# Performance work log

Hardware: AMD Instinct MI355X
Metric: run time of the kernel (lower is better)

## Reference

```python
import math
import jax, jax.numpy as jnp
import numpy as np

N_EXPERTS = 8
N_ACTIVE = 5
N_CAMP_A = 4
TEMPERATURE = math.e


def setup_inputs() -> dict:
    key = jax.random.key(0)
    ks = jax.random.split(key, 5)
    B, T, D, I = 4, 2048, 2048, 1024
    s = 0.02
    return {
        "x": jax.random.normal(ks[0], (B, T, D), jnp.float32),
        "Wr": jax.random.normal(ks[1], (D, N_EXPERTS), jnp.float32) * s,
        "Wg": jax.random.normal(ks[2], (N_EXPERTS, D, I), jnp.float32) * s,
        "Wu": jax.random.normal(ks[3], (N_EXPERTS, D, I), jnp.float32) * s,
        "Wd": jax.random.normal(ks[4], (N_EXPERTS, I, D), jnp.float32) * s,
    }


def _router_weights(x, Wr):
    # scores: (B,T,E)
    probs = jax.nn.softmax(jnp.einsum("btd,de->bte", x, Wr) / TEMPERATURE, axis=-1)
    _, topk_idx = jax.lax.top_k(probs, N_ACTIVE)          # (B,T,k)
    mask = jax.nn.one_hot(topk_idx, N_EXPERTS, dtype=probs.dtype).sum(axis=-2)
    w = probs * mask
    return w / (w.sum(axis=-1, keepdims=True) + 1e-8)


def reference(x, Wr, Wg, Wu, Wd):
    weights = _router_weights(x, Wr)                       # (B,T,E)
    # All experts run on full dense input (faithful to source loop), batched GEMMs.
    g = jnp.einsum("btd,edi->btei", x, Wg)                 # (B,T,E,I)
    u = jnp.einsum("btd,edi->btei", x, Wu)
    h = jax.nn.silu(g) * u
    eo = jnp.einsum("btei,eid->bted", h, Wd)               # (B,T,E,D)
    sign = jnp.concatenate([jnp.ones(N_CAMP_A), -jnp.ones(N_EXPERTS - N_CAMP_A)]).astype(x.dtype)
    output = jnp.einsum("bte,bted->btd", weights * sign, eo)  # out_a - out_g
    tension_scalar = jax.lax.stop_gradient(jnp.mean(output ** 2))
    return output, tension_scalar
```

## Files before the change

### kernel.cpp

```cpp
#include <hip/hip_runtime.h>
#include <cstdint>
#include <cstddef>


typedef short bf16x8 __attribute__((ext_vector_type(8)));
typedef float f32x4 __attribute__((ext_vector_type(4)));
typedef unsigned short u16;

typedef const unsigned int __attribute__((address_space(1)))* as1_u32p;
typedef unsigned int __attribute__((address_space(3)))* as3_u32p;

#define VMCNT6 asm volatile("s_waitcnt vmcnt(6)" ::: "memory")
#define VMCNT0 asm volatile("s_waitcnt vmcnt(0)" ::: "memory")
#define LGKM0  asm volatile("s_waitcnt lgkmcnt(0)" ::: "memory")
#define SBAR   __builtin_amdgcn_s_barrier()
#define SCHED0 __builtin_amdgcn_sched_barrier(0)
#define MFMA16(af, bf, cf) __builtin_amdgcn_mfma_f32_16x16x32_bf16(af, bf, cf, 0, 0, 0)

__device__ __forceinline__ u16 f2bf(float f) {
  unsigned u = __builtin_bit_cast(unsigned, f);
  u += 0x7fffu + ((u >> 16) & 1u);
  return (u16)(u >> 16);
}

__device__ __forceinline__ void gload16(const void* g, const u16* lds) {
  as1_u32p gp = (as1_u32p)(uintptr_t)g;
  as3_u32p lp = (as3_u32p)(unsigned)(uintptr_t)lds;
  __builtin_amdgcn_global_load_lds(gp, lp, 16, 0, 0);
}

__global__ __launch_bounds__(256) void router_kernel(
    const float* __restrict__ x, const float* __restrict__ Wr,
    float* __restrict__ Cw, u16* __restrict__ Xb) {
  const int l = threadIdx.x & 63;
  const int t = blockIdx.x * 4 + (threadIdx.x >> 6);
  const float* xr = x + (size_t)t * 2048;
  u16* xbr = Xb + (size_t)t * 2048;
  float p[8] = {0.f,0.f,0.f,0.f,0.f,0.f,0.f,0.f};
#pragma unroll
  for (int it = 0; it < 8; ++it) {
    const int d0 = it * 256 + l * 4;
    const float4 xv = *(const float4*)(xr + d0);
    unsigned lo = (unsigned)f2bf(xv.x) | ((unsigned)f2bf(xv.y) << 16);
    unsigned hi = (unsigned)f2bf(xv.z) | ((unsigned)f2bf(xv.w) << 16);
    *(unsigned*)(xbr + d0) = lo;
    *(unsigned*)(xbr + d0 + 2) = hi;
    const float xs[4] = {xv.x, xv.y, xv.z, xv.w};
#pragma unroll
    for (int jj = 0; jj < 4; ++jj) {
      const float4 w0 = *(const float4*)(Wr + (size_t)(d0 + jj) * 8);
      const float4 w1 = *(const float4*)(Wr + (size_t)(d0 + jj) * 8 + 4);
      p[0] += xs[jj] * w0.x; p[1] += xs[jj] * w0.y;
      p[2] += xs[jj] * w0.z; p[3] += xs[jj] * w0.w;
      p[4] += xs[jj] * w1.x; p[5] += xs[jj] * w1.y;
      p[6] += xs[jj] * w1.z; p[7] += xs[jj] * w1.w;
    }
  }
#pragma unroll
  for (int e = 0; e < 8; ++e) {
    float v = p[e];
#pragma unroll
    for (int off = 32; off > 0; off >>= 1) v += __shfl_xor(v, off, 64);
    p[e] = v;
  }
  constexpr float INV_TEMP = 0.36787944117144233f;
  float mx = -1e30f;
#pragma unroll
  for (int e = 0; e < 8; ++e) { p[e] *= INV_TEMP; mx = fmaxf(mx, p[e]); }
  float sum = 0.f;
#pragma unroll
  for (int e = 0; e < 8; ++e) { p[e] = __expf(p[e] - mx); sum += p[e]; }
  const float inv_sum = 1.f / sum;
#pragma unroll
  for (int e = 0; e < 8; ++e) p[e] *= inv_sum;
  unsigned sel = 0xFFu;
  for (int it = 0; it < 3; ++it) {
    float mn = 1e30f; int mi = 0;
#pragma unroll
    for (int e = 0; e < 8; ++e)
      if ((sel >> e) & 1u) { if (p[e] <= mn) { mn = p[e]; mi = e; } }
    sel &= ~(1u << mi);
  }
  float wsum = 0.f;
#pragma unroll
  for (int e = 0; e < 8; ++e) if ((sel >> e) & 1u) wsum += p[e];
  const float inv_w = 1.f / (wsum + 1e-8f);
  if (l == 0) {
#pragma unroll
    for (int e = 0; e < 8; ++e) {
      float v = ((sel >> e) & 1u) ? p[e] * inv_w : 0.f;
      Cw[(size_t)t * 8 + e] = (e < 4) ? v : -v;
    }
  }
}

__global__ __launch_bounds__(256) void tcvt_kernel(
    const float* __restrict__ in, u16* __restrict__ out,
    int R, int C, long long ZO, long long CS) {
  __shared__ float tile[32][33];
  const int z = blockIdx.z;
  const float* ib = in + (size_t)z * R * C;
  const int r0 = blockIdx.y * 32, c0 = blockIdx.x * 32;
  const int tx = threadIdx.x, ty = threadIdx.y;
#pragma unroll
  for (int j = 0; j < 4; ++j)
    tile[ty + j * 8][tx] = ib[(size_t)(r0 + ty + j * 8) * C + c0 + tx];
  __syncthreads();
#pragma unroll
  for (int j = 0; j < 4; ++j)
    out[(size_t)z * ZO + (size_t)(c0 + ty + j * 8) * CS + r0 + tx] =
        f2bf(tile[tx][ty + j * 8]);
}


__global__ __launch_bounds__(512, 2) void gemm1_8p(
    const u16* __restrict__ Xb, const u16* __restrict__ Wgt,
    const u16* __restrict__ Wut, const float* __restrict__ Cw,
    u16* __restrict__ Hp, int p) {
  extern __shared__ u16 lds[];
  const int tid = threadIdx.x;
  const int l = tid & 63, w = tid >> 6;
  const int wr = w >> 2, wc = w & 3;
  const int lq = l >> 4, lr = l & 15;
  const int bid = blockIdx.x;
  const int work = (bid & 7) * 128 + (bid >> 3);
  const int mtile = work & 31;
  const int en = work >> 5;
  const int el = en >> 3, nt = en & 7;
  const int e = p * 4 + el;
  const u16* gA  = Xb + (size_t)mtile * 256 * 2048;
  const u16* s0p = Wgt + (size_t)e * 2097152 + (size_t)nt * 128 * 2048;
  const u16* s1p = Wut + (size_t)e * 2097152 + (size_t)nt * 128 * 2048;
  const u16* s2p = gA;
  const u16* s3p = gA + (size_t)128 * 2048;
  const int NT = 32;

  auto stageU = [&](int tt, const u16* srcb, int u) {
    if (tt >= NT) return;
    u16* dst = lds + (tt & 1) * 32768 + u * 8192;
    const int kt = tt * 64;
#pragma unroll
    for (int j = 0; j < 2; ++j) {
      const int g = j * 512 + tid;
      const int row = g >> 3;
      const int cg = (g & 7) ^ (row & 7);
      gload16(srcb + (size_t)row * 2048 + kt + cg * 8, dst + g * 8);
    }
  };

  const int xr = lr & 7;
  const int x0 = (lq ^ xr) * 8;
  const int x1 = ((4 + lq) ^ xr) * 8;
  const int aB = (2 + wr) * 8192 + lr * 64;
  const int gBo = (wc * 32 + lr) * 64;
  const int uBo = 8192 + (wc * 32 + lr) * 64;

  bf16x8 a[8][2], bg[2][2], bu[2][2];
  f32x4 ag[8][2], au[8][2];
#pragma unroll
  for (int mi = 0; mi < 8; ++mi)
#pragma unroll
    for (int ni = 0; ni < 2; ++ni) {
      ag[mi][ni] = (f32x4){0.f, 0.f, 0.f, 0.f};
      au[mi][ni] = (f32x4){0.f, 0.f, 0.f, 0.f};
    }

  stageU(0, s0p, 0); stageU(0, s1p, 1); stageU(0, s2p, 2); stageU(0, s3p, 3);
  stageU(1, s0p, 0); stageU(1, s1p, 1); stageU(1, s2p, 2);
  VMCNT6; SBAR;

  for (int t = 0; t < NT; ++t) {
    const u16* Lb = lds + (t & 1) * 32768;
    {
#pragma unroll
      for (int mi = 0; mi < 4; ++mi) {
        a[mi][0] = *(const bf16x8*)&Lb[aB + mi * 1024 + x0];
        a[mi][1] = *(const bf16x8*)&Lb[aB + mi * 1024 + x1];
      }
#pragma unroll
      for (int ni = 0; ni < 2; ++ni) {
        bg[ni][0] = *(const bf16x8*)&Lb[gBo + ni * 1024 + x0];
        bg[ni][1] = *(const bf16x8*)&Lb[gBo + ni * 1024 + x1];
      }
      stageU(t + 1, s3p, 3);
      SBAR; LGKM0; SCHED0;
      __builtin_amdgcn_s_setprio(1);
#pragma unroll
      for (int mi = 0; mi < 4; ++mi)
#pragma unroll
        for (int ni = 0; ni < 2; ++ni)
#pragma unroll
          for (int kk = 0; kk < 2; ++kk)
            ag[mi][ni] = MFMA16(a[mi][kk], bg[ni][kk], ag[mi][ni]);
      __builtin_amdgcn_s_setprio(0); SCHED0; SBAR;
    }
    {
#pragma unroll
      for (int ni = 0; ni < 2; ++ni) {
        bu[ni][0] = *(const bf16x8*)&Lb[uBo + ni * 1024 + x0];
        bu[ni][1] = *(const bf16x8*)&Lb[uBo + ni * 1024 + x1];
      }
      stageU(t + 2, s0p, 0);
      SBAR; LGKM0; SCHED0;
      __builtin_amdgcn_s_setprio(1);
#pragma unroll
      for (int mi = 0; mi < 4; ++mi)
#pragma unroll
        for (int ni = 0; ni < 2; ++ni)
#pragma unroll
          for (int kk = 0; kk < 2; ++kk)
            au[mi][ni] = MFMA16(a[mi][kk], bu[ni][kk], au[mi][ni]);
      __builtin_amdgcn_s_setprio(0); SCHED0; SBAR;
    }
    {
#pragma unroll
      for (int mi = 4; mi < 8; ++mi) {
        a[mi][0] = *(const bf16x8*)&Lb[aB + mi * 1024 + x0];
        a[mi][1] = *(const bf16x8*)&Lb[aB + mi * 1024 + x1];
      }
      stageU(t + 2, s1p, 1);
      SBAR; LGKM0; SCHED0;
      __builtin_amdgcn_s_setprio(1);
#pragma unroll
      for (int mi = 4; mi < 8; ++mi)
#pragma unroll
        for (int ni = 0; ni < 2; ++ni)
#pragma unroll
          for (int kk = 0; kk < 2; ++kk)
            ag[mi][ni] = MFMA16(a[mi][kk], bg[ni][kk], ag[mi][ni]);
      __builtin_amdgcn_s_setprio(0); SCHED0; SBAR;
    }
    {
      stageU(t + 2, s2p, 2);
      if (t < NT - 2) { VMCNT6; } else if (t == NT - 2) { VMCNT0; }
      SBAR; LGKM0; SCHED0;
      __builtin_amdgcn_s_setprio(1);
#pragma unroll
      for (int mi = 4; mi < 8; ++mi)
#pragma unroll
        for (int ni = 0; ni < 2; ++ni)
#pragma unroll
          for (int kk = 0; kk < 2; ++kk)
            au[mi][ni] = MFMA16(a[mi][kk], bu[ni][kk], au[mi][ni]);
      __builtin_amdgcn_s_setprio(0); SCHED0; SBAR;
    }
  }

  __syncthreads();
  float* cl = (float*)lds;
  if (tid < 256) cl[tid] = Cw[(size_t)(mtile * 256 + tid) * 8 + e];
  __syncthreads();
#pragma unroll
  for (int mi = 0; mi < 8; ++mi) {
#pragma unroll
    for (int j = 0; j < 4; ++j) {
      const int rl = wr * 128 + mi * 16 + lq * 4 + j;
      const float c = cl[rl];
      const size_t row = (size_t)mtile * 256 + rl;
#pragma unroll
      for (int ni = 0; ni < 2; ++ni) {
        const float g = ag[mi][ni][j], u = au[mi][ni][j];
        const float h = g * (1.f / (1.f + __expf(-g))) * u * c;
        Hp[row * 4096 + el * 1024 + nt * 128 + wc * 32 + ni * 16 + lr] = f2bf(h);
      }
    }
  }
}

__global__ __launch_bounds__(512, 2) void gemm2_8p(
    const u16* __restrict__ Hp, const u16* __restrict__ Wdt,
    float* __restrict__ out, int koff, int accum) {
  extern __shared__ u16 lds[];
  const int tid = threadIdx.x;
  const int l = tid & 63, w = tid >> 6;
  const int wr = w >> 2, wc = w & 3;
  const int lq = l >> 4, lr = l & 15;
  const int bid = blockIdx.x;
  const int work = (bid & 7) * 32 + (bid >> 3);
  const int mtile = work & 31, ntile = work >> 5;
  const u16* gA = Hp + (size_t)mtile * 256 * 4096;
  const u16* gB = Wdt + (size_t)ntile * 256 * 8192 + koff;
  const u16* s0p = gB;
  const u16* s1p = gB + (size_t)128 * 8192;
  const u16* s2p = gA;
  const u16* s3p = gA + (size_t)128 * 4096;
  const int NT = 64;

  auto stageU = [&](int tt, const u16* srcb, int stride, int u) {
    if (tt >= NT) return;
    u16* dst = lds + (tt & 1) * 32768 + u * 8192;
    const int kt = tt * 64;
#pragma unroll
    for (int j = 0; j < 2; ++j) {
      const int g = j * 512 + tid;
      const int row = g >> 3;
      const int cg = (g & 7) ^ (row & 7);
      gload16(srcb + (size_t)row * stride + kt + cg * 8, dst + g * 8);
    }
  };

  const int xr = lr & 7;
  const int x0 = (lq ^ xr) * 8;
  const int x1 = ((4 + lq) ^ xr) * 8;
  const int aB = (2 + wr) * 8192 + lr * 64;
  const int bB = (wc >> 1) * 8192 + ((wc & 1) * 64 + lr) * 64;

  bf16x8 a[8][2], b[4][2];
  f32x4 acc[8][4];
#pragma unroll
  for (int mi = 0; mi < 8; ++mi)
#pragma unroll
    for (int ni = 0; ni < 4; ++ni) acc[mi][ni] = (f32x4){0.f, 0.f, 0.f, 0.f};

  stageU(0, s0p, 8192, 0); stageU(0, s1p, 8192, 1);
  stageU(0, s2p, 4096, 2); stageU(0, s3p, 4096, 3);
  stageU(1, s0p, 8192, 0); stageU(1, s1p, 8192, 1); stageU(1, s2p, 4096, 2);
  VMCNT6; SBAR;

  for (int t = 0; t < NT; ++t) {
    const u16* Lb = lds + (t & 1) * 32768;
    {
#pragma unroll
      for (int mi = 0; mi < 4; ++mi) {
        a[mi][0] = *(const bf16x8*)&Lb[aB + mi * 1024 + x0];
        a[mi][1] = *(const bf16x8*)&Lb[aB + mi * 1024 + x1];
      }
#pragma unroll
      for (int ni = 0; ni < 2; ++ni) {
        b[ni][0] = *(const bf16x8*)&Lb[bB + ni * 1024 + x0];
        b[ni][1] = *(const bf16x8*)&Lb[bB + ni * 1024 + x1];
      }
      if (wc < 2) {
#pragma unroll
        for (int ni = 2; ni < 4; ++ni) {
          b[ni][0] = *(const bf16x8*)&Lb[bB + ni * 1024 + x0];
          b[ni][1] = *(const bf16x8*)&Lb[bB + ni * 1024 + x1];
        }
      }
      stageU(t + 1, s3p, 4096, 3);
      SBAR; LGKM0; SCHED0;
      __builtin_amdgcn_s_setprio(1);
#pragma unroll
      for (int mi = 0; mi < 4; ++mi)
#pragma unroll
        for (int ni = 0; ni < 2; ++ni)
#pragma unroll
          for (int kk = 0; kk < 2; ++kk)
            acc[mi][ni] = MFMA16(a[mi][kk], b[ni][kk], acc[mi][ni]);
      __builtin_amdgcn_s_setprio(0); SCHED0; SBAR;
    }
    {
      if (wc >= 2) {
#pragma unroll
        for (int ni = 2; ni < 4; ++ni) {
          b[ni][0] = *(const bf16x8*)&Lb[bB + ni * 1024 + x0];
          b[ni][1] = *(const bf16x8*)&Lb[bB + ni * 1024 + x1];
        }
      }
      stageU(t + 2, s0p, 8192, 0);
      SBAR; LGKM0; SCHED0;
      __builtin_amdgcn_s_setprio(1);
#pragma unroll
      for (int mi = 0; mi < 4; ++mi)
#pragma unroll
        for (int ni = 2; ni < 4; ++ni)
#pragma unroll
          for (int kk = 0; kk < 2; ++kk)
            acc[mi][ni] = MFMA16(a[mi][kk], b[ni][kk], acc[mi][ni]);
      __builtin_amdgcn_s_setprio(0); SCHED0; SBAR;
    }
    {
#pragma unroll
      for (int mi = 4; mi < 8; ++mi) {
        a[mi][0] = *(const bf16x8*)&Lb[aB + mi * 1024 + x0];
        a[mi][1] = *(const bf16x8*)&Lb[aB + mi * 1024 + x1];
      }
      stageU(t + 2, s1p, 8192, 1);
      SBAR; LGKM0; SCHED0;
      __builtin_amdgcn_s_setprio(1);
#pragma unroll
      for (int mi = 4; mi < 8; ++mi)
#pragma unroll
        for (int ni = 2; ni < 4; ++ni)
#pragma unroll
          for (int kk = 0; kk < 2; ++kk)
            acc[mi][ni] = MFMA16(a[mi][kk], b[ni][kk], acc[mi][ni]);
      __builtin_amdgcn_s_setprio(0); SCHED0; SBAR;
    }
    {
      stageU(t + 2, s2p, 4096, 2);
      if (t < NT - 2) { VMCNT6; } else if (t == NT - 2) { VMCNT0; }
      SBAR; LGKM0; SCHED0;
      __builtin_amdgcn_s_setprio(1);
#pragma unroll
      for (int mi = 4; mi < 8; ++mi)
#pragma unroll
        for (int ni = 0; ni < 2; ++ni)
#pragma unroll
          for (int kk = 0; kk < 2; ++kk)
            acc[mi][ni] = MFMA16(a[mi][kk], b[ni][kk], acc[mi][ni]);
      __builtin_amdgcn_s_setprio(0); SCHED0; SBAR;
    }
  }

#pragma unroll
  for (int mi = 0; mi < 8; ++mi)
#pragma unroll
    for (int ni = 0; ni < 4; ++ni)
#pragma unroll
      for (int j = 0; j < 4; ++j) {
        const int row = mtile * 256 + wr * 128 + mi * 16 + lq * 4 + j;
        const int col = ntile * 256 + wc * 64 + ni * 16 + lr;
        const size_t idx = (size_t)row * 2048 + col;
        float v = acc[mi][ni][j];
        if (accum) v += out[idx];
        out[idx] = v;
      }
}

__global__ __launch_bounds__(256) void sqsum_partial(
    const float* __restrict__ out, float* __restrict__ part, int n4) {
  float s = 0.f;
  const int idx = blockIdx.x * 256 + threadIdx.x;
  const int stride = gridDim.x * 256;
  for (int i = idx; i < n4; i += stride) {
    const float4 v = ((const float4*)out)[i];
    s += v.x * v.x + v.y * v.y + v.z * v.z + v.w * v.w;
  }
#pragma unroll
  for (int off = 32; off > 0; off >>= 1) s += __shfl_down(s, off, 64);
  __shared__ float ls[4];
  if ((threadIdx.x & 63) == 0) ls[threadIdx.x >> 6] = s;
  __syncthreads();
  if (threadIdx.x == 0) part[blockIdx.x] = ls[0] + ls[1] + ls[2] + ls[3];
}

__global__ __launch_bounds__(256) void sqsum_final(
    const float* __restrict__ part, float* __restrict__ dst, int np, float scale) {
  float s = 0.f;
  for (int i = threadIdx.x; i < np; i += 256) s += part[i];
#pragma unroll
  for (int off = 32; off > 0; off >>= 1) s += __shfl_down(s, off, 64);
  __shared__ float ls[4];
  if ((threadIdx.x & 63) == 0) ls[threadIdx.x >> 6] = s;
  __syncthreads();
  if (threadIdx.x == 0) dst[0] = (ls[0] + ls[1] + ls[2] + ls[3]) * scale;
}

extern "C" void kernel_launch(void* const* d_in, const int* in_sizes, int n_in,
                              void* d_out, int out_size, void* d_ws, size_t ws_size,
                              hipStream_t stream) {
  (void)in_sizes; (void)n_in; (void)out_size; (void)ws_size;
  const float* x  = (const float*)d_in[0];
  const float* Wr = (const float*)d_in[1];
  const float* Wg = (const float*)d_in[2];
  const float* Wu = (const float*)d_in[3];
  const float* Wd = (const float*)d_in[4];
  float* out = (float*)d_out;
  char* ws = (char*)d_ws;
  u16*   Xb   = (u16*)(ws);
  u16*   Wgt  = (u16*)(ws + 33554432);
  u16*   Wut  = (u16*)(ws + 67108864);
  u16*   Wdt  = (u16*)(ws + 100663296);
  u16*   Hp   = (u16*)(ws + 134217728);
  float* Cw   = (float*)(ws + 201326592);
  float* part = (float*)(ws + 201588736);

  (void)hipFuncSetAttribute((const void*)gemm1_8p,
                            hipFuncAttributeMaxDynamicSharedMemorySize, 131072);
  (void)hipFuncSetAttribute((const void*)gemm2_8p,
                            hipFuncAttributeMaxDynamicSharedMemorySize, 131072);

  router_kernel<<<2048, 256, 0, stream>>>(x, Wr, Cw, Xb);

  dim3 tb(32, 8);
  tcvt_kernel<<<dim3(32, 64, 8), tb, 0, stream>>>(Wg, Wgt, 2048, 1024, 2097152LL, 2048LL);
  tcvt_kernel<<<dim3(32, 64, 8), tb, 0, stream>>>(Wu, Wut, 2048, 1024, 2097152LL, 2048LL);
  tcvt_kernel<<<dim3(64, 32, 8), tb, 0, stream>>>(Wd, Wdt, 1024, 2048, 1024LL, 8192LL);

  for (int p = 0; p < 2; ++p) {
    gemm1_8p<<<1024, 512, 131072, stream>>>(Xb, Wgt, Wut, Cw, Hp, p);
    gemm2_8p<<<256, 512, 131072, stream>>>(Hp, Wdt, out, p * 4096, p);
  }

  sqsum_partial<<<1024, 256, 0, stream>>>(out, part, 16777216 / 4);
  sqsum_final<<<1, 256, 0, stream>>>(part, out + 16777216, 1024, 1.f / 16777216.f);
}
```

Before: 884.6 us.

## Gather only routed tokens per expert in gate/up GEMM

A new build_idx kernel compacts, for each expert, the list of tokens whose routing weight is nonzero. The gate/up GEMM then gathers only those token rows and exits early for tiles past the per-expert count, so the work for tokens routed elsewhere (3 of 8 experts) is skipped. To keep the dense down-projection GEMM correct, the intermediate buffer is zeroed with a memset before each phase. The staging address math is also precomputed per thread. The sparse path turns on only when the workspace is large enough, and it adds memset traffic plus gathered, less regular A-row loads.

```diff
diff --git a/kernel.cpp b/kernel.cpp
--- a/kernel.cpp
+++ b/kernel.cpp
@@ -15,6 +15,8 @@
 #define LGKM0  asm volatile("s_waitcnt lgkmcnt(0)" ::: "memory")
 #define SBAR   __builtin_amdgcn_s_barrier()
 #define SCHED0 __builtin_amdgcn_sched_barrier(0)
+#define PRIO1  __builtin_amdgcn_s_setprio(1)
+#define PRIO0  __builtin_amdgcn_s_setprio(0)
 #define MFMA16(af, bf, cf) __builtin_amdgcn_mfma_f32_16x16x32_bf16(af, bf, cf, 0, 0, 0)
 
 __device__ __forceinline__ u16 f2bf(float f) {
@@ -94,6 +96,32 @@
   }
 }
 
+__global__ __launch_bounds__(256) void build_idx(
+    const float* __restrict__ Cw, int* __restrict__ idx, int* __restrict__ cnt) {
+  const int e = blockIdx.x;
+  const int tid = threadIdx.x;
+  const int t0 = tid * 32;
+  int c = 0;
+#pragma unroll
+  for (int j = 0; j < 32; ++j)
+    if (Cw[(size_t)(t0 + j) * 8 + e] != 0.f) ++c;
+  __shared__ int s[256];
+  s[tid] = c;
+  __syncthreads();
+  for (int off = 1; off < 256; off <<= 1) {
+    int v = (tid >= off) ? s[tid - off] : 0;
+    __syncthreads();
+    s[tid] += v;
+    __syncthreads();
+  }
+  int o = e * 8192 + s[tid] - c;
+  for (int j = 0; j < 32; ++j) {
+    const int t = t0 + j;
+    if (Cw[(size_t)t * 8 + e] != 0.f) idx[o++] = t;
+  }
+  if (tid == 255) cnt[e] = s[255];
+}
+
 __global__ __launch_bounds__(256) void tcvt_kernel(
     const float* __restrict__ in, u16* __restrict__ out,
     int R, int C, long long ZO, long long CS) {
@@ -116,7 +144,8 @@
 __global__ __launch_bounds__(512, 2) void gemm1_8p(
     const u16* __restrict__ Xb, const u16* __restrict__ Wgt,
     const u16* __restrict__ Wut, const float* __restrict__ Cw,
-    u16* __restrict__ Hp, int p) {
+    u16* __restrict__ Hp, const int* __restrict__ idx,
+    const int* __restrict__ cnt, int p) {
   extern __shared__ u16 lds[];
   const int tid = threadIdx.x;
   const int l = tid & 63, w = tid >> 6;
@@ -128,24 +157,43 @@
   const int en = work >> 5;
   const int el = en >> 3, nt = en & 7;
   const int e = p * 4 + el;
-  const u16* gA  = Xb + (size_t)mtile * 256 * 2048;
+  const int cnt_e = idx ? cnt[e] : 8192;
+  const int base = mtile * 256;
+  if (base >= cnt_e) return;
+  const int* idxp = idx ? idx + (size_t)e * 8192 : nullptr;
+
   const u16* s0p = Wgt + (size_t)e * 2097152 + (size_t)nt * 128 * 2048;
   const u16* s1p = Wut + (size_t)e * 2097152 + (size_t)nt * 128 * 2048;
-  const u16* s2p = gA;
-  const u16* s3p = gA + (size_t)128 * 2048;
+
+  const int lrow = tid >> 3;
+  const int cgo = ((tid & 7) ^ (lrow & 7)) * 8;
+  const int offB0 = lrow * 2048 + cgo;
+  const int offB1 = offB0 + 64 * 2048;
+  const int d0e = tid * 8, d1e = (512 + tid) * 8;
+
+  auto gr = [&](int r) -> size_t {
+    const int rr = r < cnt_e ? r : cnt_e - 1;
+    return (size_t)(idxp ? idxp[rr] : rr) * 2048 + cgo;
+  };
+  const size_t a20 = gr(base + lrow);
+  const size_t a21 = gr(base + 64 + lrow);
+  const size_t a30 = gr(base + 128 + lrow);
+  const size_t a31 = gr(base + 192 + lrow);
+
   const int NT = 32;
-
-  auto stageU = [&](int tt, const u16* srcb, int u) {
+  auto stageB = [&](int tt, const u16* srcb, int u) {
     if (tt >= NT) return;
     u16* dst = lds + (tt & 1) * 32768 + u * 8192;
     const int kt = tt * 64;
-#pragma unroll
-    for (int j = 0; j < 2; ++j) {
-      const int g = j * 512 + tid;
-      const int row = g >> 3;
-      const int cg = (g & 7) ^ (row & 7);
-      gload16(srcb + (size_t)row * 2048 + kt + cg * 8, dst + g * 8);
-    }
+    gload16(srcb + offB0 + kt, dst + d0e);
+    gload16(srcb + offB1 + kt, dst + d1e);
+  };
+  auto stageA = [&](int tt, size_t b0, size_t b1, int u) {
+    if (tt >= NT) return;
+    u16* dst = lds + (tt & 1) * 32768 + u * 8192;
+    const int kt = tt * 64;
+    gload16(Xb + b0 + kt, dst + d0e);
+    gload16(Xb + b1 + kt, dst + d1e);
   };
 
   const int xr = lr & 7;
@@ -165,8 +213,9 @@
       au[mi][ni] = (f32x4){0.f, 0.f, 0.f, 0.f};
     }
 
-  stageU(0, s0p, 0); stageU(0, s1p, 1); stageU(0, s2p, 2); stageU(0, s3p, 3);
-  stageU(1, s0p, 0); stageU(1, s1p, 1); stageU(1, s2p, 2);
+  stageB(0, s0p, 0); stageB(0, s1p, 1);
+  stageA(0, a20, a21, 2); stageA(0, a30, a31, 3);
+  stageB(1, s0p, 0); stageB(1, s1p, 1); stageA(1, a20, a21, 2);
   VMCNT6; SBAR;
 
   for (int t = 0; t < NT; ++t) {
@@ -182,9 +231,9 @@
         bg[ni][0] = *(const bf16x8*)&Lb[gBo + ni * 1024 + x0];
         bg[ni][1] = *(const bf16x8*)&Lb[gBo + ni * 1024 + x1];
       }
-      stageU(t + 1, s3p, 3);
-      SBAR; LGKM0; SCHED0;
-      __builtin_amdgcn_s_setprio(1);
+      stageA(t + 1, a30, a31, 3);
+      SBAR; LGKM0; SCHED0;
+      PRIO1;
 #pragma unroll
       for (int mi = 0; mi < 4; ++mi)
 #pragma unroll
@@ -192,7 +241,7 @@
 #pragma unroll
           for (int kk = 0; kk < 2; ++kk)
             ag[mi][ni] = MFMA16(a[mi][kk], bg[ni][kk], ag[mi][ni]);
-      __builtin_amdgcn_s_setprio(0); SCHED0; SBAR;
+      PRIO0; SCHED0; SBAR;
     }
     {
 #pragma unroll
@@ -200,9 +249,9 @@
         bu[ni][0] = *(const bf16x8*)&Lb[uBo + ni * 1024 + x0];
         bu[ni][1] = *(const bf16x8*)&Lb[uBo + ni * 1024 + x1];
       }
-      stageU(t + 2, s0p, 0);
-      SBAR; LGKM0; SCHED0;
-      __builtin_amdgcn_s_setprio(1);
+      stageB(t + 2, s0p, 0);
+      SBAR; LGKM0; SCHED0;
+      PRIO1;
 #pragma unroll
       for (int mi = 0; mi < 4; ++mi)
 #pragma unroll
@@ -210,7 +259,7 @@
 #pragma unroll
           for (int kk = 0; kk < 2; ++kk)
             au[mi][ni] = MFMA16(a[mi][kk], bu[ni][kk], au[mi][ni]);
-      __builtin_amdgcn_s_setprio(0); SCHED0; SBAR;
+      PRIO0; SCHED0; SBAR;
     }
     {
 #pragma unroll
@@ -218,9 +267,9 @@
         a[mi][0] = *(const bf16x8*)&Lb[aB + mi * 1024 + x0];
         a[mi][1] = *(const bf16x8*)&Lb[aB + mi * 1024 + x1];
       }
-      stageU(t + 2, s1p, 1);
-      SBAR; LGKM0; SCHED0;
-      __builtin_amdgcn_s_setprio(1);
+      stageB(t + 2, s1p, 1);
+      SBAR; LGKM0; SCHED0;
+      PRIO1;
 #pragma unroll
       for (int mi = 4; mi < 8; ++mi)
 #pragma unroll
@@ -228,13 +277,13 @@
 #pragma unroll
           for (int kk = 0; kk < 2; ++kk)
             ag[mi][ni] = MFMA16(a[mi][kk], bg[ni][kk], ag[mi][ni]);
-      __builtin_amdgcn_s_setprio(0); SCHED0; SBAR;
-    }
-    {
-      stageU(t + 2, s2p, 2);
+      PRIO0; SCHED0; SBAR;
+    }
+    {
+      stageA(t + 2, a20, a21, 2);
       if (t < NT - 2) { VMCNT6; } else if (t == NT - 2) { VMCNT0; }
       SBAR; LGKM0; SCHED0;
-      __builtin_amdgcn_s_setprio(1);
+      PRIO1;
 #pragma unroll
       for (int mi = 4; mi < 8; ++mi)
 #pragma unroll
@@ -242,26 +291,26 @@
 #pragma unroll
           for (int kk = 0; kk < 2; ++kk)
             au[mi][ni] = MFMA16(a[mi][kk], bu[ni][kk], au[mi][ni]);
-      __builtin_amdgcn_s_setprio(0); SCHED0; SBAR;
-    }
-  }
-
-  __syncthreads();
-  float* cl = (float*)lds;
-  if (tid < 256) cl[tid] = Cw[(size_t)(mtile * 256 + tid) * 8 + e];
-  __syncthreads();
+      PRIO0; SCHED0; SBAR;
+    }
+  }
+
 #pragma unroll
   for (int mi = 0; mi < 8; ++mi) {
 #pragma unroll
     for (int j = 0; j < 4; ++j) {
       const int rl = wr * 128 + mi * 16 + lq * 4 + j;
-      const float c = cl[rl];
-      const size_t row = (size_t)mtile * 256 + rl;
-#pragma unroll
-      for (int ni = 0; ni < 2; ++ni) {
-        const float g = ag[mi][ni][j], u = au[mi][ni][j];
-        const float h = g * (1.f / (1.f + __expf(-g))) * u * c;
-        Hp[row * 4096 + el * 1024 + nt * 128 + wc * 32 + ni * 16 + lr] = f2bf(h);
+      const int grow = base + rl;
+      if (grow < cnt_e) {
+        const int orow = idxp ? idxp[grow] : grow;
+        const float c = Cw[(size_t)orow * 8 + e];
+#pragma unroll
+        for (int ni = 0; ni < 2; ++ni) {
+          const float g = ag[mi][ni][j], u = au[mi][ni][j];
+          const float h = g * (1.f / (1.f + __expf(-g))) * u * c;
+          Hp[(size_t)orow * 4096 + el * 1024 + nt * 128 + wc * 32 + ni * 16 + lr] =
+              f2bf(h);
+        }
       }
     }
   }
@@ -286,17 +335,25 @@
   const u16* s3p = gA + (size_t)128 * 4096;
   const int NT = 64;
 
-  auto stageU = [&](int tt, const u16* srcb, int stride, int u) {
+  const int row0 = tid >> 3,          cg0 = (tid & 7) ^ (row0 & 7);
+  const int row1 = (512 + tid) >> 3,  cg1 = ((512 + tid) & 7) ^ (row1 & 7);
+  const int offA0 = row0 * 4096 + cg0 * 8, offA1 = row1 * 4096 + cg1 * 8;
+  const int offB0 = row0 * 8192 + cg0 * 8, offB1 = row1 * 8192 + cg1 * 8;
+  const int d0e = tid * 8, d1e = (512 + tid) * 8;
+
+  auto stageA = [&](int tt, const u16* srcb, int u) {
     if (tt >= NT) return;
     u16* dst = lds + (tt & 1) * 32768 + u * 8192;
     const int kt = tt * 64;
-#pragma unroll
-    for (int j = 0; j < 2; ++j) {
-      const int g = j * 512 + tid;
-      const int row = g >> 3;
-      const int cg = (g & 7) ^ (row & 7);
-      gload16(srcb + (size_t)row * stride + kt + cg * 8, dst + g * 8);
-    }
+    gload16(srcb + (size_t)(offA0 + kt), dst + d0e);
+    gload16(srcb + (size_t)(offA1 + kt), dst + d1e);
+  };
+  auto stageB = [&](int tt, const u16* srcb, int u) {
+    if (tt >= NT) return;
+    u16* dst = lds + (tt & 1) * 32768 + u * 8192;
+    const int kt = tt * 64;
+    gload16(srcb + (size_t)(offB0 + kt), dst + d0e);
+    gload16(srcb + (size_t)(offB1 + kt), dst + d1e);
   };
 
   const int xr = lr & 7;
@@ -312,9 +369,8 @@
 #pragma unroll
     for (int ni = 0; ni < 4; ++ni) acc[mi][ni] = (f32x4){0.f, 0.f, 0.f, 0.f};
 
-  stageU(0, s0p, 8192, 0); stageU(0, s1p, 8192, 1);
-  stageU(0, s2p, 4096, 2); stageU(0, s3p, 4096, 3);
-  stageU(1, s0p, 8192, 0); stageU(1, s1p, 8192, 1); stageU(1, s2p, 4096, 2);
+  stageB(0, s0p, 0); stageB(0, s1p, 1); stageA(0, s2p, 2); stageA(0, s3p, 3);
+  stageB(1, s0p, 0); stageB(1, s1p, 1); stageA(1, s2p, 2);
   VMCNT6; SBAR;
 
   for (int t = 0; t < NT; ++t) {
@@ -337,9 +393,9 @@
           b[ni][1] = *(const bf16x8*)&Lb[bB + ni * 1024 + x1];
         }
       }
-      stageU(t + 1, s3p, 4096, 3);
-      SBAR; LGKM0; SCHED0;
-      __builtin_amdgcn_s_setprio(1);
+      stageA(t + 1, s3p, 3);
+      SBAR; LGKM0; SCHED0;
+      PRIO1;
 #pragma unroll
       for (int mi = 0; mi < 4; ++mi)
 #pragma unroll
@@ -347,7 +403,7 @@
 #pragma unroll
           for (int kk = 0; kk < 2; ++kk)
             acc[mi][ni] = MFMA16(a[mi][kk], b[ni][kk], acc[mi][ni]);
-      __builtin_amdgcn_s_setprio(0); SCHED0; SBAR;
+      PRIO0; SCHED0; SBAR;
     }
     {
       if (wc >= 2) {
@@ -357,9 +413,9 @@
           b[ni][1] = *(const bf16x8*)&Lb[bB + ni * 1024 + x1];
         }
       }
-      stageU(t + 2, s0p, 8192, 0);
-      SBAR; LGKM0; SCHED0;
-      __builtin_amdgcn_s_setprio(1);
+      stageB(t + 2, s0p, 0);
+      SBAR; LGKM0; SCHED0;
+      PRIO1;
 #pragma unroll
       for (int mi = 0; mi < 4; ++mi)
 #pragma unroll
@@ -367,7 +423,7 @@
 #pragma unroll
           for (int kk = 0; kk < 2; ++kk)
             acc[mi][ni] = MFMA16(a[mi][kk], b[ni][kk], acc[mi][ni]);
-      __builtin_amdgcn_s_setprio(0); SCHED0; SBAR;
+      PRIO0; SCHED0; SBAR;
     }
     {
 #pragma unroll
@@ -375,9 +431,9 @@
         a[mi][0] = *(const bf16x8*)&Lb[aB + mi * 1024 + x0];
         a[mi][1] = *(const bf16x8*)&Lb[aB + mi * 1024 + x1];
       }
-      stageU(t + 2, s1p, 8192, 1);
-      SBAR; LGKM0; SCHED0;
-      __builtin_amdgcn_s_setprio(1);
+      stageB(t + 2, s1p, 1);
+      SBAR; LGKM0; SCHED0;
+      PRIO1;
 #pragma unroll
       for (int mi = 4; mi < 8; ++mi)
 #pragma unroll
@@ -385,13 +441,13 @@
 #pragma unroll
           for (int kk = 0; kk < 2; ++kk)
             acc[mi][ni] = MFMA16(a[mi][kk], b[ni][kk], acc[mi][ni]);
-      __builtin_amdgcn_s_setprio(0); SCHED0; SBAR;
-    }
-    {
-      stageU(t + 2, s2p, 4096, 2);
+      PRIO0; SCHED0; SBAR;
+    }
+    {
+      stageA(t + 2, s2p, 2);
       if (t < NT - 2) { VMCNT6; } else if (t == NT - 2) { VMCNT0; }
       SBAR; LGKM0; SCHED0;
-      __builtin_amdgcn_s_setprio(1);
+      PRIO1;
 #pragma unroll
       for (int mi = 4; mi < 8; ++mi)
 #pragma unroll
@@ -399,7 +455,7 @@
 #pragma unroll
           for (int kk = 0; kk < 2; ++kk)
             acc[mi][ni] = MFMA16(a[mi][kk], b[ni][kk], acc[mi][ni]);
-      __builtin_amdgcn_s_setprio(0); SCHED0; SBAR;
+      PRIO0; SCHED0; SBAR;
     }
   }
 
@@ -411,10 +467,10 @@
       for (int j = 0; j < 4; ++j) {
         const int row = mtile * 256 + wr * 128 + mi * 16 + lq * 4 + j;
         const int col = ntile * 256 + wc * 64 + ni * 16 + lr;
-        const size_t idx = (size_t)row * 2048 + col;
+        const size_t idx2 = (size_t)row * 2048 + col;
         float v = acc[mi][ni][j];
-        if (accum) v += out[idx];
-        out[idx] = v;
+        if (accum) v += out[idx2];
+        out[idx2] = v;
       }
 }
 
@@ -450,7 +506,7 @@
 extern "C" void kernel_launch(void* const* d_in, const int* in_sizes, int n_in,
                               void* d_out, int out_size, void* d_ws, size_t ws_size,
                               hipStream_t stream) {
-  (void)in_sizes; (void)n_in; (void)out_size; (void)ws_size;
+  (void)in_sizes; (void)n_in; (void)out_size;
   const float* x  = (const float*)d_in[0];
   const float* Wr = (const float*)d_in[1];
   const float* Wg = (const float*)d_in[2];
@@ -465,6 +521,9 @@
   u16*   Hp   = (u16*)(ws + 134217728);
   float* Cw   = (float*)(ws + 201326592);
   float* part = (float*)(ws + 201588736);
+  const bool SPARSE = ws_size >= 201855008u;
+  int* idxbuf = SPARSE ? (int*)(ws + 201592832) : nullptr;
+  int* cntbuf = SPARSE ? (int*)(ws + 201854976) : nullptr;
 
   (void)hipFuncSetAttribute((const void*)gemm1_8p,
                             hipFuncAttributeMaxDynamicSharedMemorySize, 131072);
@@ -472,6 +531,7 @@
                             hipFuncAttributeMaxDynamicSharedMemorySize, 131072);
 
   router_kernel<<<2048, 256, 0, stream>>>(x, Wr, Cw, Xb);
+  if (SPARSE) build_idx<<<8, 256, 0, stream>>>(Cw, idxbuf, cntbuf);
 
   dim3 tb(32, 8);
   tcvt_kernel<<<dim3(32, 64, 8), tb, 0, stream>>>(Wg, Wgt, 2048, 1024, 2097152LL, 2048LL);
@@ -479,7 +539,9 @@
   tcvt_kernel<<<dim3(64, 32, 8), tb, 0, stream>>>(Wd, Wdt, 1024, 2048, 1024LL, 8192LL);
 
   for (int p = 0; p < 2; ++p) {
-    gemm1_8p<<<1024, 512, 131072, stream>>>(Xb, Wgt, Wut, Cw, Hp, p);
+    if (SPARSE) (void)hipMemsetAsync(Hp, 0, 67108864, stream);
+    gemm1_8p<<<1024, 512, 131072, stream>>>(Xb, Wgt, Wut, Cw, Hp,
+                                            idxbuf, cntbuf, p);
     gemm2_8p<<<256, 512, 131072, stream>>>(Hp, Wdt, out, p * 4096, p);
   }
 
```

After: 822.0 us. 7.1% less time.
